# Kernel optimization log

Measured on AMD Instinct MI355X. Metric: run time of the kernel, lower is better.

The kernel has to match this reference:

```python
import jax, jax.numpy as jnp
import numpy as np

D_MODEL = 1024
NUM_HEADS = 16
D_K = D_MODEL // NUM_HEADS
ROPE_THETA = 10000.0


def apply_rope(x, pos):
    # x: [b, h, t, d], pos: [t] int
    d = x.shape[-1]
    inv_freq = 1.0 / (ROPE_THETA ** (jnp.arange(0, d, 2, dtype=jnp.float32) / d))  # [d/2]
    ang = pos.astype(jnp.float32)[:, None] * inv_freq[None, :]                     # [t, d/2]
    cos = jnp.cos(ang).astype(x.dtype)
    sin = jnp.sin(ang).astype(x.dtype)
    x1 = x[..., 0::2]  # [b,h,t,d/2]
    x2 = x[..., 1::2]
    r1 = x1 * cos - x2 * sin
    r2 = x1 * sin + x2 * cos
    return jnp.stack([r1, r2], axis=-1).reshape(x.shape)


def setup_inputs() -> dict:
    key = jax.random.key(0)
    k1, k2, k3 = jax.random.split(key, 3)
    B, T = 4, 2048
    x = jax.random.normal(k1, (B, T, D_MODEL), dtype=jnp.float32)
    W_qkv = jax.random.normal(k2, (D_MODEL, 3 * D_MODEL), dtype=jnp.float32) * 0.02
    W_o = jax.random.normal(k3, (D_MODEL, D_MODEL), dtype=jnp.float32) * 0.02
    token_positions = jnp.arange(T, dtype=jnp.int32)
    return {"x": x, "W_qkv": W_qkv, "W_o": W_o, "token_positions": token_positions}


def reference(x, W_qkv, W_o, token_positions):
    B, T, _ = x.shape
    H, Dk = NUM_HEADS, D_K
    qkv = x @ W_qkv                                   # [b, t, 3*d_model]
    qkv = qkv.reshape(B, T, 3, H, Dk)                 # last dim ordered (qkv, h, d)
    qkv = jnp.transpose(qkv, (2, 0, 3, 1, 4))         # [3, b, h, t, d]
    q, k, v = qkv[0], qkv[1], qkv[2]
    q = apply_rope(q, token_positions)
    k = apply_rope(k, token_positions)
    scale = 1.0 / jnp.sqrt(jnp.asarray(Dk, dtype=x.dtype))
    scores = jnp.einsum('bhqd,bhkd->bhqk', q, k) * scale
    causal = jnp.tril(jnp.ones((T, T), dtype=bool))
    scores = jnp.where(causal, scores, jnp.asarray(-jnp.inf, dtype=scores.dtype))
    attn = jax.nn.softmax(scores, axis=-1)
    vals = jnp.einsum('bhqk,bhkd->bhqd', attn, v)     # [b, h, t, d]
    out = jnp.transpose(vals, (0, 2, 1, 3)).reshape(B, T, H * Dk)
    return out @ W_o
```

## Files before the change

kernel.cpp:

```cpp
#include <hip/hip_runtime.h>
#include <math.h>

#define B_  4
#define T_  2048
#define DM  1024
#define H_  16
#define DK  64
#define N3  3072

typedef __attribute__((ext_vector_type(8))) __bf16 bf16x8;
typedef __attribute__((ext_vector_type(4))) float f32x4;
typedef __attribute__((ext_vector_type(4))) unsigned int u32x4;

static __device__ __forceinline__ unsigned int f2bf(float f) {
    union { float f; unsigned int u; } v; v.f = f;
    return (v.u + 0x7fffu + ((v.u >> 16) & 1u)) >> 16;
}
static __device__ __forceinline__ unsigned int pack2bf(float a, float b) {
    return f2bf(a) | (f2bf(b) << 16);
}
static __device__ __forceinline__ void gload_lds16(const void* g, void* l) {
    __builtin_amdgcn_global_load_lds(
        (const __attribute__((address_space(1))) unsigned int*)g,
        (__attribute__((address_space(3))) unsigned int*)l, 16, 0, 0);
}

__global__ __launch_bounds__(256)
void convert_copy(const float* __restrict__ src, unsigned short* __restrict__ dst, int n8)
{
    const int i = blockIdx.x * 256 + threadIdx.x;
    if (i >= n8) return;
    const float4 f0 = ((const float4*)src)[i * 2];
    const float4 f1 = ((const float4*)src)[i * 2 + 1];
    u32x4 wv;
    wv.x = pack2bf(f0.x, f0.y); wv.y = pack2bf(f0.z, f0.w);
    wv.z = pack2bf(f1.x, f1.y); wv.w = pack2bf(f1.z, f1.w);
    ((u32x4*)dst)[i] = wv;
}

__global__ __launch_bounds__(256)
void convert_T(const float* __restrict__ src, unsigned short* __restrict__ dst, int K, int N)
{
    __shared__ float tile[32][33];
    const int n0 = blockIdx.x * 32, k0 = blockIdx.y * 32;
    const int tid = threadIdx.x;
    #pragma unroll
    for (int p = 0; p < 4; ++p) {
        const int idx = p * 256 + tid;
        const int r = idx >> 5, c = idx & 31;
        tile[r][c] = src[(size_t)(k0 + r) * N + n0 + c];
    }
    __syncthreads();
    #pragma unroll
    for (int p = 0; p < 4; ++p) {
        const int idx = p * 256 + tid;
        const int r = idx >> 5, c = idx & 31;
        dst[(size_t)(n0 + r) * K + k0 + c] = (unsigned short)f2bf(tile[c][r]);
    }
}

__global__ __launch_bounds__(256)
void rope_table(const int* __restrict__ pos, float2* __restrict__ RC)
{
    const int i = blockIdx.x * 256 + threadIdx.x;
    const int t = i >> 5, dp = i & 31;
    const float ifr = __powf(10000.0f, -(float)(2 * dp) * (1.0f / 64.0f));
    float s, c;
    __sincosf((float)pos[t] * ifr, &s, &c);
    RC[i] = make_float2(c, s);
}

__global__ __launch_bounds__(256, 3)
void qkv_rope_kernel(const unsigned short* __restrict__ xb,
                     const unsigned short* __restrict__ WT,
                     const float2* __restrict__ RC,
                     unsigned short* __restrict__ Qb,
                     unsigned short* __restrict__ Kb,
                     unsigned short* __restrict__ Vtb)
{
    __shared__ u32x4 Asv[3][512];
    __shared__ u32x4 Bsv[3][512];
    const int tid  = threadIdx.x;
    const int lin  = blockIdx.x;
    const int xcd  = lin & 7;
    const int idx  = lin >> 3;
    const int col0 = (xcd * 3 + (idx % 3)) * 128;
    const int row0 = (idx / 3) * 128;
    const int l = tid & 63, w = tid >> 6;
    const int wr = w >> 1, wc = w & 1;
    const int lr = l & 15, hi4 = l >> 4;

    const int srow = tid & 127;
    const int kel  = (tid >> 7) * 8;
    const size_t a0 = (size_t)(row0 + srow) * DM + kel;
    const size_t b0 = (size_t)(col0 + srow) * DM + kel;

    f32x4 acc[4][4];
    #pragma unroll
    for (int m = 0; m < 4; ++m)
        #pragma unroll
        for (int n = 0; n < 4; ++n)
            acc[m][n] = (f32x4){0.f, 0.f, 0.f, 0.f};

    gload_lds16(&xb[a0],      &Asv[0][tid]);
    gload_lds16(&xb[a0 + 16], &Asv[0][256 + tid]);
    gload_lds16(&WT[b0],      &Bsv[0][tid]);
    gload_lds16(&WT[b0 + 16], &Bsv[0][256 + tid]);
    gload_lds16(&xb[a0 + 32], &Asv[1][tid]);
    gload_lds16(&xb[a0 + 48], &Asv[1][256 + tid]);
    gload_lds16(&WT[b0 + 32], &Bsv[1][tid]);
    gload_lds16(&WT[b0 + 48], &Bsv[1][256 + tid]);
    asm volatile("s_waitcnt vmcnt(4)" ::: "memory");
    __builtin_amdgcn_s_barrier();

    #pragma unroll 1
    for (int it = 0; it < 32; ++it) {
        const int cur = it % 3;
        const bool more = (it + 2 < 32);
        if (more) {
            const int nb = (it + 2) % 3;
            const int kn = (it + 2) * 32;
            gload_lds16(&xb[a0 + kn],      &Asv[nb][tid]);
            gload_lds16(&xb[a0 + kn + 16], &Asv[nb][256 + tid]);
            gload_lds16(&WT[b0 + kn],      &Bsv[nb][tid]);
            gload_lds16(&WT[b0 + kn + 16], &Bsv[nb][256 + tid]);
        }
        u32x4 a[4], b[4];
        #pragma unroll
        for (int m = 0; m < 4; ++m) a[m] = Asv[cur][hi4 * 128 + wr * 64 + m * 16 + lr];
        #pragma unroll
        for (int n = 0; n < 4; ++n) b[n] = Bsv[cur][hi4 * 128 + wc * 64 + n * 16 + lr];
        #pragma unroll
        for (int m = 0; m < 4; ++m)
            #pragma unroll
            for (int n = 0; n < 4; ++n)
                acc[m][n] = __builtin_amdgcn_mfma_f32_16x16x32_bf16(
                    __builtin_bit_cast(bf16x8, a[m]),
                    __builtin_bit_cast(bf16x8, b[n]),
                    acc[m][n], 0, 0, 0);
        if (more) asm volatile("s_waitcnt vmcnt(4)" ::: "memory");
        else      asm volatile("s_waitcnt vmcnt(0)" ::: "memory");
        __builtin_amdgcn_s_barrier();
    }

    const int which = col0 >> 10;
    const int h     = ((col0 & 1023) >> 6) + wc;
    const int bb    = row0 >> 11;
    const int t0w   = (row0 & 2047) + wr * 64;

    if (which == 2) {
        #pragma unroll
        for (int n = 0; n < 4; ++n) {
            const int d = n * 16 + lr;
            #pragma unroll
            for (int m = 0; m < 4; ++m) {
                uint2 val;
                val.x = pack2bf(acc[m][n][0], acc[m][n][1]);
                val.y = pack2bf(acc[m][n][2], acc[m][n][3]);
                *(uint2*)&Vtb[((size_t)(bb * H_ + h) * DK + d) * T_ + t0w + m * 16 + hi4 * 4] = val;
            }
        }
    } else {
        unsigned short* dst = (which == 0) ? Qb : Kb;
        const float postscale = (which == 0) ? 0.125f : 1.0f;
        #pragma unroll
        for (int n = 0; n < 4; ++n) {
            const int d  = n * 16 + lr;
            const int dp = d >> 1;
            #pragma unroll
            for (int m = 0; m < 4; ++m)
                #pragma unroll
                for (int r = 0; r < 4; ++r) {
                    const int t = t0w + m * 16 + hi4 * 4 + r;
                    const float v = acc[m][n][r];
                    const float partner = __shfl_xor(v, 1, 64);
                    const float2 cs = RC[t * 32 + dp];
                    const float rv = ((d & 1) ? (partner * cs.y + v * cs.x)
                                              : (v * cs.x - partner * cs.y)) * postscale;
                    dst[((size_t)(bb * H_ + h) * T_ + t) * DK + d] = (unsigned short)f2bf(rv);
                }
        }
    }
}

__global__ __launch_bounds__(512)
void flash_attn_kernel(const unsigned short* __restrict__ Qg,
                       const unsigned short* __restrict__ Kg,
                       const unsigned short* __restrict__ Vtg,
                       unsigned short* __restrict__ Og)
{
    __shared__ u32x4 K4[512];
    __shared__ u32x4 Vt4[512];
    __shared__ unsigned int Pex[8][16 * 36];

    const int tid = threadIdx.x;
    const int l = tid & 63, w = tid >> 6;
    const int lr = l & 15, hi4 = l >> 4;
    const int lin = blockIdx.x;
    const int qt  = 7 - (lin >> 6);
    const int g   = lin & 63;
    const int h   = g & 15, b = g >> 4;
    const int q0 = qt * 256;
    const size_t hb = (size_t)(b * H_ + h) * T_ * DK;
    unsigned int* pw = &Pex[w][0];

    const int srow = tid >> 3, scc = tid & 7;
    const int sdst = srow * 8 + (scc ^ (srow & 7));

    u32x4 qf[2][2];
    #pragma unroll
    for (int m = 0; m < 2; ++m)
        #pragma unroll
        for (int ks = 0; ks < 2; ++ks)
            qf[m][ks] = *(const u32x4*)&Qg[hb + (size_t)(q0 + w * 32 + m * 16 + lr) * DK
                                           + ks * 32 + hi4 * 8];

    f32x4 acc_ot[2][4];
    float m_i[2], l_i[2];
    #pragma unroll
    for (int m = 0; m < 2; ++m) {
        m_i[m] = -INFINITY; l_i[m] = 0.f;
        #pragma unroll
        for (int df = 0; df < 4; ++df) acc_ot[m][df] = (f32x4){0.f, 0.f, 0.f, 0.f};
    }

    const int qwave = q0 + w * 32;
    const int nkt = (q0 >> 6) + 4;

    u32x4 kr = *(const u32x4*)&Kg [hb + (size_t)srow * DK + scc * 8];
    u32x4 vr = *(const u32x4*)&Vtg[hb + (size_t)srow * T_ + scc * 8];

    for (int kt = 0; kt < nkt; ++kt) {
        const int kv0 = kt * 64;
        __syncthreads();
        K4[sdst] = kr; Vt4[sdst] = vr;
        __syncthreads();
        if (kt + 1 < nkt) {
            const int kvn = kv0 + 64;
            kr = *(const u32x4*)&Kg [hb + (size_t)(kvn + srow) * DK + scc * 8];
            vr = *(const u32x4*)&Vtg[hb + (size_t)srow * T_ + kvn + scc * 8];
        }
        if (kv0 > qwave + 31) continue;

        f32x4 st[2][4];
        #pragma unroll
        for (int m = 0; m < 2; ++m)
            #pragma unroll
            for (int nf = 0; nf < 4; ++nf)
                st[m][nf] = (f32x4){0.f, 0.f, 0.f, 0.f};
        #pragma unroll
        for (int ks = 0; ks < 2; ++ks) {
            u32x4 kb4[4];
            #pragma unroll
            for (int nf = 0; nf < 4; ++nf) {
                const int row = nf * 16 + lr;
                kb4[nf] = K4[row * 8 + ((ks * 4 + hi4) ^ (row & 7))];
            }
            #pragma unroll
            for (int m = 0; m < 2; ++m)
                #pragma unroll
                for (int nf = 0; nf < 4; ++nf)
                    st[m][nf] = __builtin_amdgcn_mfma_f32_16x16x32_bf16(
                        __builtin_bit_cast(bf16x8, kb4[nf]),
                        __builtin_bit_cast(bf16x8, qf[m][ks]), st[m][nf], 0, 0, 0);
        }

        const bool needmask = (kv0 + 63 > qwave);
        u32x4 pfrag[2][2];
        #pragma unroll
        for (int m = 0; m < 2; ++m) {
            const int qg = qwave + m * 16 + lr;
            float sv[4][4];
            #pragma unroll
            for (int nf = 0; nf < 4; ++nf)
                #pragma unroll
                for (int r = 0; r < 4; ++r) {
                    float xv = st[m][nf][r];
                    if (needmask && (kv0 + nf * 16 + hi4 * 4 + r) > qg) xv = -INFINITY;
                    sv[nf][r] = xv;
                }
            float mx = sv[0][0];
            #pragma unroll
            for (int nf = 0; nf < 4; ++nf)
                #pragma unroll
                for (int r = 0; r < 4; ++r) mx = fmaxf(mx, sv[nf][r]);
            mx = fmaxf(mx, __shfl_xor(mx, 16, 64));
            mx = fmaxf(mx, __shfl_xor(mx, 32, 64));
            const bool defer = __all((m_i[m] > -1e30f) && (mx <= m_i[m] + 2.0f));
            if (!defer) {
                const float mnew = fmaxf(m_i[m], mx);
                const float alpha = __expf(m_i[m] - mnew);
                m_i[m] = mnew;
                l_i[m] *= alpha;
                #pragma unroll
                for (int df = 0; df < 4; ++df) acc_ot[m][df] *= alpha;
            }
            float p[4][4], rs = 0.f;
            #pragma unroll
            for (int nf = 0; nf < 4; ++nf)
                #pragma unroll
                for (int r = 0; r < 4; ++r) {
                    p[nf][r] = __expf(sv[nf][r] - m_i[m]);
                    rs += p[nf][r];
                }
            rs += __shfl_xor(rs, 16, 64);
            rs += __shfl_xor(rs, 32, 64);
            l_i[m] += rs;
            #pragma unroll
            for (int nf = 0; nf < 4; ++nf) {
                uint2 pr;
                pr.x = pack2bf(p[nf][0], p[nf][1]);
                pr.y = pack2bf(p[nf][2], p[nf][3]);
                *(uint2*)&pw[lr * 36 + nf * 8 + hi4 * 2] = pr;
            }
            #pragma unroll
            for (int ks = 0; ks < 2; ++ks)
                pfrag[m][ks] = *(const u32x4*)&pw[lr * 36 + ks * 16 + hi4 * 4];
        }

        #pragma unroll
        for (int ks = 0; ks < 2; ++ks) {
            u32x4 vb[4];
            #pragma unroll
            for (int df = 0; df < 4; ++df) {
                const int d = df * 16 + lr;
                vb[df] = Vt4[d * 8 + ((ks * 4 + hi4) ^ (d & 7))];
            }
            #pragma unroll
            for (int m = 0; m < 2; ++m)
                #pragma unroll
                for (int df = 0; df < 4; ++df)
                    acc_ot[m][df] = __builtin_amdgcn_mfma_f32_16x16x32_bf16(
                        __builtin_bit_cast(bf16x8, vb[df]),
                        __builtin_bit_cast(bf16x8, pfrag[m][ks]), acc_ot[m][df], 0, 0, 0);
        }
    }

    #pragma unroll
    for (int m = 0; m < 2; ++m) {
        const float inv = 1.0f / l_i[m];
        #pragma unroll
        for (int df = 0; df < 4; ++df) {
            uint2 pr;
            pr.x = pack2bf(acc_ot[m][df][0] * inv, acc_ot[m][df][1] * inv);
            pr.y = pack2bf(acc_ot[m][df][2] * inv, acc_ot[m][df][3] * inv);
            *(uint2*)&pw[lr * 36 + df * 8 + hi4 * 2] = pr;
        }
        #pragma unroll
        for (int ks2 = 0; ks2 < 2; ++ks2) {
            const u32x4 ov = *(const u32x4*)&pw[lr * 36 + ks2 * 16 + hi4 * 4];
            *(u32x4*)&Og[hb + (size_t)(qwave + m * 16 + lr) * DK + ks2 * 32 + hi4 * 8] = ov;
        }
    }
}

__global__ __launch_bounds__(256, 3)
void out_proj_kernel(const unsigned short* __restrict__ Ob,
                     const unsigned short* __restrict__ WoT,
                     float* __restrict__ out)
{
    __shared__ u32x4 Asv[3][512];
    __shared__ u32x4 Bsv[3][512];
    const int tid  = threadIdx.x;
    const int lin  = blockIdx.x;
    const int col0 = (lin & 7) * 128;
    const int row0 = (lin >> 3) * 128;
    const int l = tid & 63, w = tid >> 6;
    const int wr = w >> 1, wc = w & 1;
    const int lr = l & 15, hi4 = l >> 4;
    const int bb = row0 >> 11, trow0 = row0 & 2047;

    const int srow = tid & 127;
    const int kel  = (tid >> 7) * 8;
    const size_t bsrc = (size_t)(col0 + srow) * DM + kel;
    auto asrc = [&](int k) -> size_t {
        const int hh = k >> 6, dd = k & 63;
        return ((size_t)(bb * H_ + hh) * T_ + trow0 + srow) * DK + dd;
    };

    f32x4 acc[4][4];
    #pragma unroll
    for (int m = 0; m < 4; ++m)
        #pragma unroll
        for (int n = 0; n < 4; ++n)
            acc[m][n] = (f32x4){0.f, 0.f, 0.f, 0.f};

    gload_lds16(&Ob[asrc(kel)],           &Asv[0][tid]);
    gload_lds16(&Ob[asrc(kel + 16)],      &Asv[0][256 + tid]);
    gload_lds16(&WoT[bsrc],               &Bsv[0][tid]);
    gload_lds16(&WoT[bsrc + 16],          &Bsv[0][256 + tid]);
    gload_lds16(&Ob[asrc(32 + kel)],      &Asv[1][tid]);
    gload_lds16(&Ob[asrc(32 + kel + 16)], &Asv[1][256 + tid]);
    gload_lds16(&WoT[bsrc + 32],          &Bsv[1][tid]);
    gload_lds16(&WoT[bsrc + 48],          &Bsv[1][256 + tid]);
    asm volatile("s_waitcnt vmcnt(4)" ::: "memory");
    __builtin_amdgcn_s_barrier();

    #pragma unroll 1
    for (int it = 0; it < 32; ++it) {
        const int cur = it % 3;
        const bool more = (it + 2 < 32);
        if (more) {
            const int nb = (it + 2) % 3;
            const int kn = (it + 2) * 32;
            gload_lds16(&Ob[asrc(kn + kel)],      &Asv[nb][tid]);
            gload_lds16(&Ob[asrc(kn + kel + 16)], &Asv[nb][256 + tid]);
            gload_lds16(&WoT[bsrc + kn],          &Bsv[nb][tid]);
            gload_lds16(&WoT[bsrc + kn + 16],     &Bsv[nb][256 + tid]);
        }
        u32x4 a[4], b[4];
        #pragma unroll
        for (int m = 0; m < 4; ++m) a[m] = Asv[cur][hi4 * 128 + wr * 64 + m * 16 + lr];
        #pragma unroll
        for (int n = 0; n < 4; ++n) b[n] = Bsv[cur][hi4 * 128 + wc * 64 + n * 16 + lr];
        #pragma unroll
        for (int m = 0; m < 4; ++m)
            #pragma unroll
            for (int n = 0; n < 4; ++n)
                acc[m][n] = __builtin_amdgcn_mfma_f32_16x16x32_bf16(
                    __builtin_bit_cast(bf16x8, a[m]),
                    __builtin_bit_cast(bf16x8, b[n]),
                    acc[m][n], 0, 0, 0);
        if (more) asm volatile("s_waitcnt vmcnt(4)" ::: "memory");
        else      asm volatile("s_waitcnt vmcnt(0)" ::: "memory");
        __builtin_amdgcn_s_barrier();
    }

    #pragma unroll
    for (int n = 0; n < 4; ++n) {
        const int gc = col0 + wc * 64 + n * 16 + lr;
        #pragma unroll
        for (int m = 0; m < 4; ++m)
            #pragma unroll
            for (int r = 0; r < 4; ++r)
                out[(size_t)(row0 + wr * 64 + m * 16 + hi4 * 4 + r) * DM + gc] = acc[m][n][r];
    }
}

extern "C" void kernel_launch(void* const* d_in, const int* in_sizes, int n_in,
                              void* d_out, int out_size, void* d_ws, size_t ws_size,
                              hipStream_t stream)
{
    const float* x    = (const float*)d_in[0];
    const float* Wqkv = (const float*)d_in[1];
    const float* Wo   = (const float*)d_in[2];
    const int*   pos  = (const int*)d_in[3];
    float* out = (float*)d_out;

    unsigned short* ws    = (unsigned short*)d_ws;
    unsigned short* xb    = ws;
    unsigned short* WqkvT = xb    + 8388608;
    unsigned short* WoT   = WqkvT + 3145728;
    unsigned short* Qb    = WoT   + 1048576;
    unsigned short* Kb    = Qb    + 8388608;
    unsigned short* Vtb   = Kb    + 8388608;
    unsigned short* Ob    = Vtb   + 8388608;
    float2*         RC    = (float2*)(Ob + 8388608);

    convert_copy<<<dim3(4096), 256, 0, stream>>>(x, xb, 1048576);
    convert_T<<<dim3(96, 32), 256, 0, stream>>>(Wqkv, WqkvT, 1024, 3072);
    convert_T<<<dim3(32, 32), 256, 0, stream>>>(Wo, WoT, 1024, 1024);
    rope_table<<<dim3(256), 256, 0, stream>>>(pos, RC);
    qkv_rope_kernel<<<dim3(1536), 256, 0, stream>>>(xb, WqkvT, RC, Qb, Kb, Vtb);
    flash_attn_kernel<<<dim3(512), 512, 0, stream>>>(Qb, Kb, Vtb, Ob);
    out_proj_kernel<<<dim3(512), 256, 0, stream>>>(Ob, WoT, out);
}
```

Measured before the change: 254.7 us.

## Triple-buffer K/V tiles in flash attention with direct global-to-LDS async loads

The flash attention kernel now streams K and V^T tiles straight into LDS with global_load_lds instead of staging them through registers. A three-slot ring buffer keeps two tiles in flight, and a vmcnt wait plus one barrier per iteration replaces the two __syncthreads. The aim is to hide global load latency behind MFMA and softmax work and to cut register pressure and barrier count. The cost is three times the K/V LDS footprint, which may lower occupancy. The swizzle moves from the LDS destination to the global source address.

```diff
diff --git a/kernel.cpp b/kernel.cpp
--- a/kernel.cpp
+++ b/kernel.cpp
@@ -189,8 +189,8 @@
                        const unsigned short* __restrict__ Vtg,
                        unsigned short* __restrict__ Og)
 {
-    __shared__ u32x4 K4[512];
-    __shared__ u32x4 Vt4[512];
+    __shared__ u32x4 K4[3][512];
+    __shared__ u32x4 Vt4[3][512];
     __shared__ unsigned int Pex[8][16 * 36];
 
     const int tid = threadIdx.x;
@@ -204,8 +204,10 @@
     const size_t hb = (size_t)(b * H_ + h) * T_ * DK;
     unsigned int* pw = &Pex[w][0];
 
-    const int srow = tid >> 3, scc = tid & 7;
-    const int sdst = srow * 8 + (scc ^ (srow & 7));
+    const int slotrow = tid >> 3;
+    const int csrc    = (tid & 7) ^ (slotrow & 7);
+    const size_t ksrc0 = hb + (size_t)slotrow * DK + csrc * 8;
+    const size_t vsrc0 = hb + (size_t)slotrow * T_ + csrc * 8;
 
     u32x4 qf[2][2];
     #pragma unroll
@@ -227,113 +229,123 @@
     const int qwave = q0 + w * 32;
     const int nkt = (q0 >> 6) + 4;
 
-    u32x4 kr = *(const u32x4*)&Kg [hb + (size_t)srow * DK + scc * 8];
-    u32x4 vr = *(const u32x4*)&Vtg[hb + (size_t)srow * T_ + scc * 8];
-
+    gload_lds16(&Kg [ksrc0],            &K4[0][tid]);
+    gload_lds16(&Vtg[vsrc0],            &Vt4[0][tid]);
+    gload_lds16(&Kg [ksrc0 + 64 * DK],  &K4[1][tid]);
+    gload_lds16(&Vtg[vsrc0 + 64],       &Vt4[1][tid]);
+    asm volatile("s_waitcnt vmcnt(2)" ::: "memory");
+    __builtin_amdgcn_s_barrier();
+
+    #pragma unroll 1
     for (int kt = 0; kt < nkt; ++kt) {
         const int kv0 = kt * 64;
-        __syncthreads();
-        K4[sdst] = kr; Vt4[sdst] = vr;
-        __syncthreads();
-        if (kt + 1 < nkt) {
-            const int kvn = kv0 + 64;
-            kr = *(const u32x4*)&Kg [hb + (size_t)(kvn + srow) * DK + scc * 8];
-            vr = *(const u32x4*)&Vtg[hb + (size_t)srow * T_ + kvn + scc * 8];
-        }
-        if (kv0 > qwave + 31) continue;
-
-        f32x4 st[2][4];
-        #pragma unroll
-        for (int m = 0; m < 2; ++m)
-            #pragma unroll
-            for (int nf = 0; nf < 4; ++nf)
-                st[m][nf] = (f32x4){0.f, 0.f, 0.f, 0.f};
-        #pragma unroll
-        for (int ks = 0; ks < 2; ++ks) {
-            u32x4 kb4[4];
-            #pragma unroll
-            for (int nf = 0; nf < 4; ++nf) {
-                const int row = nf * 16 + lr;
-                kb4[nf] = K4[row * 8 + ((ks * 4 + hi4) ^ (row & 7))];
+        const int cur = kt % 3;
+        const bool more = (kt + 2 < nkt);
+        if (more) {
+            const int nb = (kt + 2) % 3;
+            const int kvn = kv0 + 128;
+            gload_lds16(&Kg [ksrc0 + (size_t)kvn * DK], &K4[nb][tid]);
+            gload_lds16(&Vtg[vsrc0 + kvn],              &Vt4[nb][tid]);
+        }
+
+        if (kv0 <= qwave + 31) {
+            f32x4 st[2][4];
+            #pragma unroll
+            for (int m = 0; m < 2; ++m)
+                #pragma unroll
+                for (int nf = 0; nf < 4; ++nf)
+                    st[m][nf] = (f32x4){0.f, 0.f, 0.f, 0.f};
+            #pragma unroll
+            for (int ks = 0; ks < 2; ++ks) {
+                u32x4 kb4[4];
+                #pragma unroll
+                for (int nf = 0; nf < 4; ++nf) {
+                    const int row = nf * 16 + lr;
+                    kb4[nf] = K4[cur][row * 8 + ((ks * 4 + hi4) ^ (row & 7))];
+                }
+                #pragma unroll
+                for (int m = 0; m < 2; ++m)
+                    #pragma unroll
+                    for (int nf = 0; nf < 4; ++nf)
+                        st[m][nf] = __builtin_amdgcn_mfma_f32_16x16x32_bf16(
+                            __builtin_bit_cast(bf16x8, kb4[nf]),
+                            __builtin_bit_cast(bf16x8, qf[m][ks]), st[m][nf], 0, 0, 0);
             }
-            #pragma unroll
-            for (int m = 0; m < 2; ++m)
+
+            const bool needmask = (kv0 + 63 > qwave);
+            u32x4 pfrag[2][2];
+            #pragma unroll
+            for (int m = 0; m < 2; ++m) {
+                const int qg = qwave + m * 16 + lr;
+                float sv[4][4];
                 #pragma unroll
                 for (int nf = 0; nf < 4; ++nf)
-                    st[m][nf] = __builtin_amdgcn_mfma_f32_16x16x32_bf16(
-                        __builtin_bit_cast(bf16x8, kb4[nf]),
-                        __builtin_bit_cast(bf16x8, qf[m][ks]), st[m][nf], 0, 0, 0);
-        }
-
-        const bool needmask = (kv0 + 63 > qwave);
-        u32x4 pfrag[2][2];
-        #pragma unroll
-        for (int m = 0; m < 2; ++m) {
-            const int qg = qwave + m * 16 + lr;
-            float sv[4][4];
-            #pragma unroll
-            for (int nf = 0; nf < 4; ++nf)
-                #pragma unroll
-                for (int r = 0; r < 4; ++r) {
-                    float xv = st[m][nf][r];
-                    if (needmask && (kv0 + nf * 16 + hi4 * 4 + r) > qg) xv = -INFINITY;
-                    sv[nf][r] = xv;
+                    #pragma unroll
+                    for (int r = 0; r < 4; ++r) {
+                        float xv = st[m][nf][r];
+                        if (needmask && (kv0 + nf * 16 + hi4 * 4 + r) > qg) xv = -INFINITY;
+                        sv[nf][r] = xv;
+                    }
+                float mx = sv[0][0];
+                #pragma unroll
+                for (int nf = 0; nf < 4; ++nf)
+                    #pragma unroll
+                    for (int r = 0; r < 4; ++r) mx = fmaxf(mx, sv[nf][r]);
+                mx = fmaxf(mx, __shfl_xor(mx, 16, 64));
+                mx = fmaxf(mx, __shfl_xor(mx, 32, 64));
+                const bool defer = __all((m_i[m] > -1e30f) && (mx <= m_i[m] + 2.0f));
+                if (!defer) {
+                    const float mnew = fmaxf(m_i[m], mx);
+                    const float alpha = __expf(m_i[m] - mnew);
+                    m_i[m] = mnew;
+                    l_i[m] *= alpha;
+                    #pragma unroll
+                    for (int df = 0; df < 4; ++df) acc_ot[m][df] *= alpha;
                 }
-            float mx = sv[0][0];
-            #pragma unroll
-            for (int nf = 0; nf < 4; ++nf)
-                #pragma unroll
-                for (int r = 0; r < 4; ++r) mx = fmaxf(mx, sv[nf][r]);
-            mx = fmaxf(mx, __shfl_xor(mx, 16, 64));
-            mx = fmaxf(mx, __shfl_xor(mx, 32, 64));
-            const bool defer = __all((m_i[m] > -1e30f) && (mx <= m_i[m] + 2.0f));
-            if (!defer) {
-                const float mnew = fmaxf(m_i[m], mx);
-                const float alpha = __expf(m_i[m] - mnew);
-                m_i[m] = mnew;
-                l_i[m] *= alpha;
-                #pragma unroll
-                for (int df = 0; df < 4; ++df) acc_ot[m][df] *= alpha;
+                float p[4][4], rs = 0.f;
+                #pragma unroll
+                for (int nf = 0; nf < 4; ++nf)
+                    #pragma unroll
+                    for (int r = 0; r < 4; ++r) {
+                        p[nf][r] = __expf(sv[nf][r] - m_i[m]);
+                        rs += p[nf][r];
+                    }
+                rs += __shfl_xor(rs, 16, 64);
+                rs += __shfl_xor(rs, 32, 64);
+                l_i[m] += rs;
+                #pragma unroll
+                for (int nf = 0; nf < 4; ++nf) {
+                    uint2 pr;
+                    pr.x = pack2bf(p[nf][0], p[nf][1]);
+                    pr.y = pack2bf(p[nf][2], p[nf][3]);
+                    *(uint2*)&pw[lr * 36 + nf * 8 + hi4 * 2] = pr;
+                }
+                #pragma unroll
+                for (int ks = 0; ks < 2; ++ks)
+                    pfrag[m][ks] = *(const u32x4*)&pw[lr * 36 + ks * 16 + hi4 * 4];
             }
-            float p[4][4], rs = 0.f;
-            #pragma unroll
-            for (int nf = 0; nf < 4; ++nf)
-                #pragma unroll
-                for (int r = 0; r < 4; ++r) {
-                    p[nf][r] = __expf(sv[nf][r] - m_i[m]);
-                    rs += p[nf][r];
+
+            #pragma unroll
+            for (int ks = 0; ks < 2; ++ks) {
+                u32x4 vb[4];
+                #pragma unroll
+                for (int df = 0; df < 4; ++df) {
+                    const int d = df * 16 + lr;
+                    vb[df] = Vt4[cur][d * 8 + ((ks * 4 + hi4) ^ (d & 7))];
                 }
-            rs += __shfl_xor(rs, 16, 64);
-            rs += __shfl_xor(rs, 32, 64);
-            l_i[m] += rs;
-            #pragma unroll
-            for (int nf = 0; nf < 4; ++nf) {
-                uint2 pr;
-                pr.x = pack2bf(p[nf][0], p[nf][1]);
-                pr.y = pack2bf(p[nf][2], p[nf][3]);
-                *(uint2*)&pw[lr * 36 + nf * 8 + hi4 * 2] = pr;
+                #pragma unroll
+                for (int m = 0; m < 2; ++m)
+                    #pragma unroll
+                    for (int df = 0; df < 4; ++df)
+                        acc_ot[m][df] = __builtin_amdgcn_mfma_f32_16x16x32_bf16(
+                            __builtin_bit_cast(bf16x8, vb[df]),
+                            __builtin_bit_cast(bf16x8, pfrag[m][ks]), acc_ot[m][df], 0, 0, 0);
             }
-            #pragma unroll
-            for (int ks = 0; ks < 2; ++ks)
-                pfrag[m][ks] = *(const u32x4*)&pw[lr * 36 + ks * 16 + hi4 * 4];
-        }
-
-        #pragma unroll
-        for (int ks = 0; ks < 2; ++ks) {
-            u32x4 vb[4];
-            #pragma unroll
-            for (int df = 0; df < 4; ++df) {
-                const int d = df * 16 + lr;
-                vb[df] = Vt4[d * 8 + ((ks * 4 + hi4) ^ (d & 7))];
-            }
-            #pragma unroll
-            for (int m = 0; m < 2; ++m)
-                #pragma unroll
-                for (int df = 0; df < 4; ++df)
-                    acc_ot[m][df] = __builtin_amdgcn_mfma_f32_16x16x32_bf16(
-                        __builtin_bit_cast(bf16x8, vb[df]),
-                        __builtin_bit_cast(bf16x8, pfrag[m][ks]), acc_ot[m][df], 0, 0, 0);
-        }
+        }
+
+        if (more) asm volatile("s_waitcnt vmcnt(2)" ::: "memory");
+        else      asm volatile("s_waitcnt vmcnt(0)" ::: "memory");
+        __builtin_amdgcn_s_barrier();
     }
 
     #pragma unroll
```

Result: slower. 267.8 us (+5.1%).
